# Kernel tuning notes

Measured on AMD Instinct MI355X. Metric: run time of the kernel, lower is better.

The kernel has to match this reference:

```python
import jax, jax.numpy as jnp
import numpy as np

D_MODEL = 1024
D_EXPERT = 1024
NUM_EXPERTS = 8
TOP_K = 2


def setup_inputs() -> dict:
    key = jax.random.key(0)
    k_x, k_r, k1, k2, k3 = jax.random.split(key, 5)
    scale = 0.02
    x = jax.random.normal(k_x, (4, 2048, D_MODEL), dtype=jnp.float32)
    Wr = jax.random.normal(k_r, (D_MODEL, NUM_EXPERTS), dtype=jnp.float32) * scale
    # stacked per-expert SwiGLU weights (Linear with bias=False)
    W1 = jax.random.normal(k1, (NUM_EXPERTS, D_MODEL, D_EXPERT), dtype=jnp.float32) * scale
    W2 = jax.random.normal(k2, (NUM_EXPERTS, D_EXPERT, D_MODEL), dtype=jnp.float32) * scale
    W3 = jax.random.normal(k3, (NUM_EXPERTS, D_MODEL, D_EXPERT), dtype=jnp.float32) * scale
    return {"x": x, "Wr": Wr, "W1": W1, "W2": W2, "W3": W3}


def reference(x, Wr, W1, W2, W3):
    B, T, C = x.shape
    xf = x.reshape(-1, C)                       # [N, C], N = B*T
    logits = xf @ Wr                            # [N, E]
    probs = jax.nn.softmax(logits, axis=-1)
    topk_p, topk_i = jax.lax.top_k(probs, TOP_K)  # [N, K]
    topk_p = topk_p / jnp.sum(topk_p, axis=-1, keepdims=True)
    out = jnp.zeros_like(xf)
    for e in range(NUM_EXPERTS):
        # combine weight per token for this expert (0 if not routed here)
        w_e = jnp.sum(topk_p * (topk_i == e), axis=-1)  # [N]
        h = jax.nn.silu(xf @ W1[e]) * (xf @ W3[e])       # [N, d_expert]
        y = h @ W2[e]                                    # [N, C]
        out = out + w_e[:, None] * y
    return out.reshape(B, T, C)
```

## Files before the change

### kernel.cpp

```cpp
#include <hip/hip_runtime.h>
#include <hip/hip_bf16.h>

typedef __attribute__((ext_vector_type(8))) short short8;
typedef __attribute__((ext_vector_type(4))) short short4v;
typedef __attribute__((ext_vector_type(4))) unsigned short ushort4v;
typedef __attribute__((ext_vector_type(4))) float f32x4;

#define NTOK 8192
#define DM 1024
#define DE 1024
#define NE 8

__device__ __forceinline__ float bf2f(unsigned short u) {
  union { unsigned int i; float f; } v; v.i = ((unsigned int)u) << 16; return v.f;
}
__device__ __forceinline__ unsigned short f2bf(float f) {
  union { float f; unsigned int i; } v; v.f = f;
  unsigned int lsb = (v.i >> 16) & 1;
  v.i += 0x7fffu + lsb;
  return (unsigned short)(v.i >> 16);
}
__device__ __forceinline__ void gl_lds(const short* g, short* l) {
  __builtin_amdgcn_global_load_lds((const __attribute__((address_space(1))) void*)g,
                                   (__attribute__((address_space(3))) void*)l, 16, 0, 0);
}

__global__ __launch_bounds__(256) void k_transw(const float* __restrict__ W1,
                                                const float* __restrict__ W2,
                                                const float* __restrict__ W3,
                                                short* __restrict__ wcat,
                                                short* __restrict__ w2t) {
  __shared__ float t[64][65];
  int mid = blockIdx.z;
  const float* src;
  if (mid < 8)       src = W1 + (size_t)mid * (DM * DE);
  else if (mid < 16) src = W3 + (size_t)(mid - 8) * (DM * DE);
  else               src = W2 + (size_t)(mid - 16) * (DE * DM);
  int tid = threadIdx.x;
  int tr = tid >> 4, tc = tid & 15;
  int kbase = blockIdx.y * 64, nbase = blockIdx.x * 64;
#pragma unroll
  for (int j = 0; j < 4; j++) {
    int kr = tr + j * 16;
    f32x4 v = *(const f32x4*)(src + (size_t)(kbase + kr) * 1024 + nbase + tc * 4);
    t[kr][tc * 4 + 0] = v[0]; t[kr][tc * 4 + 1] = v[1];
    t[kr][tc * 4 + 2] = v[2]; t[kr][tc * 4 + 3] = v[3];
  }
  __syncthreads();
#pragma unroll
  for (int j = 0; j < 4; j++) {
    int n = tr + j * 16;
    int ng = nbase + n;
    short4v o;
    o[0] = (short)f2bf(t[tc * 4 + 0][n]);
    o[1] = (short)f2bf(t[tc * 4 + 1][n]);
    o[2] = (short)f2bf(t[tc * 4 + 2][n]);
    o[3] = (short)f2bf(t[tc * 4 + 3][n]);
    size_t dsto;
    if (mid < 16) {
      int e = mid & 7, p = mid >> 3;
      int row_out = ((ng >> 7) * 256) + p * 128 + (ng & 127);
      dsto = (size_t)e * (2048 * 1024) + (size_t)row_out * 1024 + kbase + tc * 4;
      *(short4v*)(wcat + dsto) = o;
    } else {
      int e = mid - 16;
      dsto = (size_t)e * (1024 * 1024) + (size_t)ng * 1024 + kbase + tc * 4;
      *(short4v*)(w2t + dsto) = o;
    }
  }
}

__global__ __launch_bounds__(256) void k_router(const float* __restrict__ x,
                                                const float* __restrict__ Wr,
                                                short* __restrict__ xb,
                                                int* __restrict__ esel,
                                                float* __restrict__ wgt) {
  int wid = threadIdx.x >> 6, lane = threadIdx.x & 63;
  int t = blockIdx.x * 4 + wid;
  const float* xr = x + (size_t)t * DM;
  float acc[8];
#pragma unroll
  for (int e = 0; e < 8; e++) acc[e] = 0.f;
#pragma unroll
  for (int i = 0; i < 4; i++) {
    int kb = (i * 64 + lane) * 4;
    f32x4 v = *(const f32x4*)(xr + kb);
    ushort4v ob;
#pragma unroll
    for (int j = 0; j < 4; j++) {
      f32x4 w0 = *(const f32x4*)(Wr + (size_t)(kb + j) * 8);
      f32x4 w1 = *(const f32x4*)(Wr + (size_t)(kb + j) * 8 + 4);
      float xv = v[j];
      ob[j] = f2bf(xv);
      acc[0] += xv * w0[0]; acc[1] += xv * w0[1];
      acc[2] += xv * w0[2]; acc[3] += xv * w0[3];
      acc[4] += xv * w1[0]; acc[5] += xv * w1[1];
      acc[6] += xv * w1[2]; acc[7] += xv * w1[3];
    }
    *(ushort4v*)(xb + (size_t)t * DM + kb) = ob;
  }
#pragma unroll
  for (int off = 32; off; off >>= 1)
#pragma unroll
    for (int e = 0; e < 8; e++) acc[e] += __shfl_xor(acc[e], off);
  float m0 = -1e30f, m1 = -1e30f; int e0 = 0, e1 = 0;
#pragma unroll
  for (int e = 0; e < 8; e++) {
    float v = acc[e];
    if (v > m0) { m1 = m0; e1 = e0; m0 = v; e0 = e; }
    else if (v > m1) { m1 = v; e1 = e; }
  }
  float p = __expf(m1 - m0);
  if (lane == 0) {
    esel[2 * t] = e0; esel[2 * t + 1] = e1;
    wgt[2 * t] = 1.f / (1.f + p); wgt[2 * t + 1] = p / (1.f + p);
  }
}

__global__ __launch_bounds__(256) void k_rank(const int* __restrict__ esel,
                                              int* __restrict__ cnt,
                                              int* __restrict__ rank) {
  __shared__ int wcnt[4][8];
  __shared__ int woff[4][8];
  int tid = threadIdx.x;
  int lane = tid & 63, wid = tid >> 6;
  int t = blockIdx.x * 256 + tid;
  int e0 = esel[2 * t], e1 = esel[2 * t + 1];
  unsigned long long lt = (lane == 0) ? 0ull : ((~0ull) >> (64 - lane));
  int r0 = 0, r1 = 0;
#pragma unroll
  for (int e = 0; e < 8; e++) {
    unsigned long long m0 = __ballot(e0 == e);
    unsigned long long m1 = __ballot(e1 == e);
    int c0 = __popcll(m0);
    if (e0 == e) r0 = __popcll(m0 & lt);
    if (e1 == e) r1 = c0 + __popcll(m1 & lt);
    if (lane == 0) wcnt[wid][e] = c0 + __popcll(m1);
  }
  __syncthreads();
  if (tid < 8) {
    int e = tid;
    int c0 = wcnt[0][e], c1 = wcnt[1][e], c2 = wcnt[2][e], c3 = wcnt[3][e];
    int base = atomicAdd(&cnt[e], c0 + c1 + c2 + c3);
    woff[0][e] = base;
    woff[1][e] = base + c0;
    woff[2][e] = base + c0 + c1;
    woff[3][e] = base + c0 + c1 + c2;
  }
  __syncthreads();
  rank[2 * t] = woff[wid][e0] + r0;
  rank[2 * t + 1] = woff[wid][e1] + r1;
}

__global__ void k_offsets(const int* __restrict__ cnt, int* __restrict__ off) {
  if (threadIdx.x == 0) {
    int s = 0;
    for (int e = 0; e < NE; e++) { off[e] = s; s += cnt[e]; }
  }
}

__global__ __launch_bounds__(256) void k_scatter(const int* __restrict__ off,
                                                 const int* __restrict__ esel,
                                                 const int* __restrict__ rank,
                                                 int* __restrict__ tok_of_slot,
                                                 int* __restrict__ slot_of_tok) {
  int t = blockIdx.x * 256 + threadIdx.x;
#pragma unroll
  for (int j = 0; j < 2; j++) {
    int e = esel[2 * t + j];
    int s = off[e] + rank[2 * t + j];
    tok_of_slot[s] = t;
    slot_of_tok[2 * t + j] = s;
  }
}

template<int FFN1>
__global__ __launch_bounds__(512, 2) void k_ffn(const short* __restrict__ Abase,
                                                const short* __restrict__ Bbase,
                                                const int* __restrict__ cnt,
                                                const int* __restrict__ off,
                                                const int* __restrict__ tok_of_slot,
                                                short* __restrict__ outp) {
  const int e = blockIdx.y;
  const int cnt_e = cnt[e];
  const int m0 = blockIdx.z * 256;
  if (m0 >= cnt_e) return;
  const int bse = off[e];
  const int nt = blockIdx.x;
  const short* Bt = Bbase + (size_t)e * ((FFN1 ? 2048 : 1024) * 1024) + (size_t)(nt * 256) * 1024;

  __shared__ __align__(128) short Al[2][16384];
  __shared__ __align__(128) short Bl[2][16384];

  const int tid = threadIdx.x;
  const int lane = tid & 63, wid = tid >> 6;
  const int wr = wid >> 2, wcn = wid & 3;

  const short* srcA[4]; const short* srcB[4];
#pragma unroll
  for (int p = 0; p < 4; p++) {
    int r = p * 64 + (tid >> 3);
    int sc = (tid & 7) ^ (r & 7);
    int rowA = m0 + r; if (rowA >= cnt_e) rowA = cnt_e - 1;
    long ar = FFN1 ? (long)tok_of_slot[bse + rowA] : (long)(bse + rowA);
    srcA[p] = Abase + ar * 1024 + sc * 8;
    srcB[p] = Bt + (size_t)r * 1024 + sc * 8;
  }

  int aoff[8], boff[4];
#pragma unroll
  for (int m = 0; m < 8; m++) {
    int r = wr * 128 + m * 16 + (lane & 15);
    aoff[m] = r * 128 + (((lane >> 4) ^ (r & 7)) * 16);
  }
#pragma unroll
  for (int n = 0; n < 4; n++) {
    int rb = FFN1 ? (wcn * 32 + (n & 1) * 16 + (n >> 1) * 128 + (lane & 15))
                  : (wcn * 64 + n * 16 + (lane & 15));
    boff[n] = rb * 128 + (((lane >> 4) ^ (rb & 7)) * 16);
  }

  f32x4 acc[8][4];
#pragma unroll
  for (int m = 0; m < 8; m++)
#pragma unroll
    for (int n = 0; n < 4; n++) acc[m][n] = (f32x4){0.f, 0.f, 0.f, 0.f};

#pragma unroll
  for (int p = 0; p < 4; p++) gl_lds(srcA[p], &Al[0][p * 4096 + wid * 512]);
#pragma unroll
  for (int p = 0; p < 4; p++) gl_lds(srcB[p], &Bl[0][p * 4096 + wid * 512]);
  asm volatile("s_waitcnt vmcnt(0)" ::: "memory");
  __builtin_amdgcn_s_barrier();

  int cur = 0;
  for (int t = 0; t < 16; ++t) {
    const int nxt = cur ^ 1;
    const int ktn = (t + 1 < 16) ? (t + 1) : 15;
    const char* Ab = (const char*)Al[cur];
    const char* Bb = (const char*)Bl[cur];
    short8 a[4], b[4];
#pragma unroll
    for (int i = 0; i < 4; i++) a[i] = *(const short8*)(Ab + aoff[i]);
#pragma unroll
    for (int i = 0; i < 4; i++) b[i] = *(const short8*)(Bb + boff[i]);
#pragma unroll
    for (int p = 0; p < 4; p++) gl_lds(srcA[p] + ktn * 64, &Al[nxt][p * 4096 + wid * 512]);
    __builtin_amdgcn_s_setprio(1);
#pragma unroll
    for (int m = 0; m < 4; m++)
#pragma unroll
      for (int n = 0; n < 4; n++)
        acc[m][n] = __builtin_amdgcn_mfma_f32_16x16x32_bf16(a[m], b[n], acc[m][n], 0, 0, 0);
#pragma unroll
    for (int i = 0; i < 4; i++) a[i] = *(const short8*)(Ab + aoff[4 + i]);
#pragma unroll
    for (int p = 0; p < 4; p++) gl_lds(srcB[p] + ktn * 64, &Bl[nxt][p * 4096 + wid * 512]);
#pragma unroll
    for (int m = 0; m < 4; m++)
#pragma unroll
      for (int n = 0; n < 4; n++)
        acc[m + 4][n] = __builtin_amdgcn_mfma_f32_16x16x32_bf16(a[m], b[n], acc[m + 4][n], 0, 0, 0);
#pragma unroll
    for (int i = 0; i < 4; i++) a[i] = *(const short8*)(Ab + (aoff[i] ^ 64));
#pragma unroll
    for (int i = 0; i < 4; i++) b[i] = *(const short8*)(Bb + (boff[i] ^ 64));
#pragma unroll
    for (int m = 0; m < 4; m++)
#pragma unroll
      for (int n = 0; n < 4; n++)
        acc[m][n] = __builtin_amdgcn_mfma_f32_16x16x32_bf16(a[m], b[n], acc[m][n], 0, 0, 0);
#pragma unroll
    for (int i = 0; i < 4; i++) a[i] = *(const short8*)(Ab + (aoff[4 + i] ^ 64));
#pragma unroll
    for (int m = 0; m < 4; m++)
#pragma unroll
      for (int n = 0; n < 4; n++)
        acc[m + 4][n] = __builtin_amdgcn_mfma_f32_16x16x32_bf16(a[m], b[n], acc[m + 4][n], 0, 0, 0);
    __builtin_amdgcn_s_setprio(0);
    asm volatile("s_waitcnt vmcnt(0)" ::: "memory");
    __builtin_amdgcn_s_barrier();
    cur = nxt;
  }

  if (FFN1) {
#pragma unroll
    for (int m = 0; m < 8; m++)
#pragma unroll
      for (int cc = 0; cc < 2; cc++) {
        f32x4 v1 = acc[m][cc], v3 = acc[m][cc + 2];
        int col = nt * 128 + wcn * 32 + cc * 16 + (lane & 15);
#pragma unroll
        for (int i = 0; i < 4; i++) {
          int row = m0 + wr * 128 + m * 16 + ((lane >> 4) * 4) + i;
          if (row < cnt_e) {
            float a1v = v1[i];
            float hv = (a1v / (1.f + __expf(-a1v))) * v3[i];
            outp[(size_t)(bse + row) * DE + col] = (short)f2bf(hv);
          }
        }
      }
  } else {
#pragma unroll
    for (int m = 0; m < 8; m++)
#pragma unroll
      for (int n = 0; n < 4; n++) {
        f32x4 v = acc[m][n];
        int col = nt * 256 + wcn * 64 + n * 16 + (lane & 15);
#pragma unroll
        for (int i = 0; i < 4; i++) {
          int row = m0 + wr * 128 + m * 16 + ((lane >> 4) * 4) + i;
          if (row < cnt_e)
            outp[(size_t)(bse + row) * DM + col] = (short)f2bf(v[i]);
        }
      }
  }
}

__global__ __launch_bounds__(256) void k_combine(const short* __restrict__ y,
                                                 const int* __restrict__ slot_of_tok,
                                                 const float* __restrict__ wgt,
                                                 float* __restrict__ out) {
  int t = blockIdx.x;
  int s0 = slot_of_tok[2 * t], s1 = slot_of_tok[2 * t + 1];
  float w0 = wgt[2 * t], w1 = wgt[2 * t + 1];
  int c = threadIdx.x * 4;
  short4v a = *(const short4v*)(y + (size_t)s0 * DM + c);
  short4v b = *(const short4v*)(y + (size_t)s1 * DM + c);
  f32x4 o;
#pragma unroll
  for (int j = 0; j < 4; j++)
    o[j] = w0 * bf2f((unsigned short)a[j]) + w1 * bf2f((unsigned short)b[j]);
  *(f32x4*)(out + (size_t)t * DM + c) = o;
}

extern "C" void kernel_launch(void* const* d_in, const int* in_sizes, int n_in,
                              void* d_out, int out_size, void* d_ws, size_t ws_size,
                              hipStream_t stream) {
  const float* x  = (const float*)d_in[0];
  const float* Wr = (const float*)d_in[1];
  const float* W1 = (const float*)d_in[2];
  const float* W2 = (const float*)d_in[3];
  const float* W3 = (const float*)d_in[4];
  float* out = (float*)d_out;
  char* ws = (char*)d_ws;

  short* xb   = (short*)(ws);
  short* wcat = (short*)(ws + 16777216);
  short* w2t  = (short*)(ws + 50331648);
  short* h    = (short*)(ws + 67108864);
  short* y    = (short*)(ws + 100663296);
  char* meta = ws + 134217728;
  int* cnt          = (int*)(meta);
  int* off          = (int*)(meta + 256);
  int* esel         = (int*)(meta + 512);
  int* rank         = (int*)(meta + 512 + 65536);
  int* tok_of_slot  = (int*)(meta + 512 + 2 * 65536);
  int* slot_of_tok  = (int*)(meta + 512 + 3 * 65536);
  float* wgt        = (float*)(meta + 512 + 4 * 65536);

  hipMemsetAsync(cnt, 0, 32, stream);
  k_transw<<<dim3(16, 16, 24), 256, 0, stream>>>(W1, W2, W3, wcat, w2t);
  k_router<<<2048, 256, 0, stream>>>(x, Wr, xb, esel, wgt);
  k_rank<<<32, 256, 0, stream>>>(esel, cnt, rank);
  k_offsets<<<1, 64, 0, stream>>>(cnt, off);
  k_scatter<<<32, 256, 0, stream>>>(off, esel, rank, tok_of_slot, slot_of_tok);
  k_ffn<1><<<dim3(8, 8, 32), 512, 0, stream>>>(xb, wcat, cnt, off, tok_of_slot, h);
  k_ffn<0><<<dim3(4, 8, 32), 512, 0, stream>>>(h, w2t, cnt, off, tok_of_slot, y);
  k_combine<<<8192, 256, 0, stream>>>(y, slot_of_tok, wgt, out);
}
```

Baseline: 261.9 us.

## Split GEMM tiles into half-tile stages with finer-grained async LDS prefetch

Restructures the expert GEMM main loop so A and B tiles are loaded in halves, with partial vmcnt waits instead of a full drain each K-step. Loads for the next and next-next K-step are interleaved with MFMA blocks, and the first half-buffer is refilled as soon as it has been consumed. The warp-to-tile mapping is also interleaved (rows strided by 32 across warps, columns by 64), and the epilogue index math is updated to match. The aim is to hide global-to-LDS latency behind compute and keep the MFMA pipe busy. The cost is more barriers per step and careful vmcnt accounting that could race if miscounted.

```diff
diff --git a/kernel.cpp b/kernel.cpp
--- a/kernel.cpp
+++ b/kernel.cpp
@@ -196,29 +196,26 @@
   const int lane = tid & 63, wid = tid >> 6;
   const int wr = wid >> 2, wcn = wid & 3;
 
-  const short* srcA[4]; const short* srcB[4];
-#pragma unroll
-  for (int p = 0; p < 4; p++) {
-    int r = p * 64 + (tid >> 3);
-    int sc = (tid & 7) ^ (r & 7);
-    int rowA = m0 + r; if (rowA >= cnt_e) rowA = cnt_e - 1;
-    long ar = FFN1 ? (long)tok_of_slot[bse + rowA] : (long)(bse + rowA);
-    srcA[p] = Abase + ar * 1024 + sc * 8;
-    srcB[p] = Bt + (size_t)r * 1024 + sc * 8;
-  }
-
-  int aoff[8], boff[4];
-#pragma unroll
-  for (int m = 0; m < 8; m++) {
-    int r = wr * 128 + m * 16 + (lane & 15);
-    aoff[m] = r * 128 + (((lane >> 4) ^ (r & 7)) * 16);
-  }
-#pragma unroll
-  for (int n = 0; n < 4; n++) {
-    int rb = FFN1 ? (wcn * 32 + (n & 1) * 16 + (n >> 1) * 128 + (lane & 15))
-                  : (wcn * 64 + n * 16 + (lane & 15));
-    boff[n] = rb * 128 + (((lane >> 4) ^ (rb & 7)) * 16);
-  }
+  const int sc = ((lane & 7) ^ (lane >> 3)) * 8;
+  const short* srcA[2][2];
+  const short* srcB[2];
+#pragma unroll
+  for (int j = 0; j < 2; j++) {
+#pragma unroll
+    for (int h = 0; h < 2; h++) {
+      int r = h * 128 + (wid * 2 + j) * 8 + (lane >> 3);
+      int row = m0 + r; if (row >= cnt_e) row = cnt_e - 1;
+      long ar = FFN1 ? (long)tok_of_slot[bse + row] : (long)(bse + row);
+      srcA[j][h] = Abase + ar * 1024 + sc;
+    }
+    srcB[j] = Bt + (size_t)((wid * 2 + j) * 8 + (lane >> 3)) * 1024 + sc;
+  }
+
+  const int chnk = ((lane >> 4) ^ (lane & 7)) * 16;
+  const int aB0 = (wr * 16 + (lane & 15)) * 128 + chnk;
+  const int aB1 = aB0 ^ 64;
+  const int bB0 = (wcn * 16 + (lane & 15)) * 128 + chnk;
+  const int bB1 = bB0 ^ 64;
 
   f32x4 acc[8][4];
 #pragma unroll
@@ -226,73 +223,78 @@
 #pragma unroll
     for (int n = 0; n < 4; n++) acc[m][n] = (f32x4){0.f, 0.f, 0.f, 0.f};
 
-#pragma unroll
-  for (int p = 0; p < 4; p++) gl_lds(srcA[p], &Al[0][p * 4096 + wid * 512]);
-#pragma unroll
-  for (int p = 0; p < 4; p++) gl_lds(srcB[p], &Bl[0][p * 4096 + wid * 512]);
+#define STG_A(b, h, kt) { \
+    gl_lds(srcA[0][h] + (kt) * 64, &Al[b][(h) * 8192 + (wid * 2 + 0) * 512]); \
+    gl_lds(srcA[1][h] + (kt) * 64, &Al[b][(h) * 8192 + (wid * 2 + 1) * 512]); }
+#define STG_B(b, h, kt) { \
+    gl_lds(srcB[0] + (h) * 131072 + (kt) * 64, &Bl[b][(h) * 8192 + (wid * 2 + 0) * 512]); \
+    gl_lds(srcB[1] + (h) * 131072 + (kt) * 64, &Bl[b][(h) * 8192 + (wid * 2 + 1) * 512]); }
+
+  STG_A(0, 0, 0); STG_B(0, 0, 0); STG_B(0, 1, 0); STG_A(0, 1, 0);
+  STG_A(1, 0, 1); STG_B(1, 0, 1);
+
+#define KTBODY(KT, BUF) { \
+    const int kA = ((KT) + 1 < 16) ? (KT) + 1 : 15; \
+    const int kB = ((KT) + 2 < 16) ? (KT) + 2 : 15; \
+    const char* pA = (const char*)(&Al[BUF][0]); \
+    const char* pB = (const char*)(&Bl[BUF][0]); \
+    short8 a[4], b0[4], b1[4]; \
+     \
+    asm volatile("s_waitcnt vmcnt(6)" ::: "memory"); \
+    __builtin_amdgcn_s_barrier(); \
+    _Pragma("unroll") for (int m = 0; m < 4; m++) a[m] = *(const short8*)(pA + aB0 + m * 4096); \
+    _Pragma("unroll") for (int n = 0; n < 4; n++) b0[n] = *(const short8*)(pB + bB0 + (n & 1) * 8192 + (n >> 1) * 16384); \
+    STG_B(BUF ^ 1, 1, kA); \
+    __builtin_amdgcn_s_setprio(1); \
+    _Pragma("unroll") for (int m = 0; m < 4; m++) \
+      _Pragma("unroll") for (int n = 0; n < 4; n++) \
+        acc[m][n] = __builtin_amdgcn_mfma_f32_16x16x32_bf16(a[m], b0[n], acc[m][n], 0, 0, 0); \
+    __builtin_amdgcn_s_setprio(0); \
+     \
+    _Pragma("unroll") for (int m = 0; m < 4; m++) a[m] = *(const short8*)(pA + aB1 + m * 4096); \
+    _Pragma("unroll") for (int n = 0; n < 4; n++) b1[n] = *(const short8*)(pB + bB1 + (n & 1) * 8192 + (n >> 1) * 16384); \
+    STG_A(BUF ^ 1, 1, kA); \
+    __builtin_amdgcn_s_setprio(1); \
+    _Pragma("unroll") for (int m = 0; m < 4; m++) \
+      _Pragma("unroll") for (int n = 0; n < 4; n++) \
+        acc[m][n] = __builtin_amdgcn_mfma_f32_16x16x32_bf16(a[m], b1[n], acc[m][n], 0, 0, 0); \
+    __builtin_amdgcn_s_setprio(0); \
+     \
+    asm volatile("s_waitcnt vmcnt(8)" ::: "memory"); \
+    __builtin_amdgcn_s_barrier(); \
+    _Pragma("unroll") for (int m = 0; m < 4; m++) a[m] = *(const short8*)(pA + aB0 + 16384 + m * 4096); \
+    STG_A(BUF, 0, kB); \
+    __builtin_amdgcn_s_setprio(1); \
+    _Pragma("unroll") for (int m = 0; m < 4; m++) \
+      _Pragma("unroll") for (int n = 0; n < 4; n++) \
+        acc[m + 4][n] = __builtin_amdgcn_mfma_f32_16x16x32_bf16(a[m], b0[n], acc[m + 4][n], 0, 0, 0); \
+    __builtin_amdgcn_s_setprio(0); \
+     \
+    _Pragma("unroll") for (int m = 0; m < 4; m++) a[m] = *(const short8*)(pA + aB1 + 16384 + m * 4096); \
+    STG_B(BUF, 0, kB); \
+    __builtin_amdgcn_s_setprio(1); \
+    _Pragma("unroll") for (int m = 0; m < 4; m++) \
+      _Pragma("unroll") for (int n = 0; n < 4; n++) \
+        acc[m + 4][n] = __builtin_amdgcn_mfma_f32_16x16x32_bf16(a[m], b1[n], acc[m + 4][n], 0, 0, 0); \
+    __builtin_amdgcn_s_setprio(0); \
+  }
+
+  for (int kt2 = 0; kt2 < 16; kt2 += 2) {
+    KTBODY(kt2, 0);
+    KTBODY(kt2 + 1, 1);
+  }
   asm volatile("s_waitcnt vmcnt(0)" ::: "memory");
-  __builtin_amdgcn_s_barrier();
-
-  int cur = 0;
-  for (int t = 0; t < 16; ++t) {
-    const int nxt = cur ^ 1;
-    const int ktn = (t + 1 < 16) ? (t + 1) : 15;
-    const char* Ab = (const char*)Al[cur];
-    const char* Bb = (const char*)Bl[cur];
-    short8 a[4], b[4];
-#pragma unroll
-    for (int i = 0; i < 4; i++) a[i] = *(const short8*)(Ab + aoff[i]);
-#pragma unroll
-    for (int i = 0; i < 4; i++) b[i] = *(const short8*)(Bb + boff[i]);
-#pragma unroll
-    for (int p = 0; p < 4; p++) gl_lds(srcA[p] + ktn * 64, &Al[nxt][p * 4096 + wid * 512]);
-    __builtin_amdgcn_s_setprio(1);
-#pragma unroll
-    for (int m = 0; m < 4; m++)
-#pragma unroll
-      for (int n = 0; n < 4; n++)
-        acc[m][n] = __builtin_amdgcn_mfma_f32_16x16x32_bf16(a[m], b[n], acc[m][n], 0, 0, 0);
-#pragma unroll
-    for (int i = 0; i < 4; i++) a[i] = *(const short8*)(Ab + aoff[4 + i]);
-#pragma unroll
-    for (int p = 0; p < 4; p++) gl_lds(srcB[p] + ktn * 64, &Bl[nxt][p * 4096 + wid * 512]);
-#pragma unroll
-    for (int m = 0; m < 4; m++)
-#pragma unroll
-      for (int n = 0; n < 4; n++)
-        acc[m + 4][n] = __builtin_amdgcn_mfma_f32_16x16x32_bf16(a[m], b[n], acc[m + 4][n], 0, 0, 0);
-#pragma unroll
-    for (int i = 0; i < 4; i++) a[i] = *(const short8*)(Ab + (aoff[i] ^ 64));
-#pragma unroll
-    for (int i = 0; i < 4; i++) b[i] = *(const short8*)(Bb + (boff[i] ^ 64));
-#pragma unroll
-    for (int m = 0; m < 4; m++)
-#pragma unroll
-      for (int n = 0; n < 4; n++)
-        acc[m][n] = __builtin_amdgcn_mfma_f32_16x16x32_bf16(a[m], b[n], acc[m][n], 0, 0, 0);
-#pragma unroll
-    for (int i = 0; i < 4; i++) a[i] = *(const short8*)(Ab + (aoff[4 + i] ^ 64));
-#pragma unroll
-    for (int m = 0; m < 4; m++)
-#pragma unroll
-      for (int n = 0; n < 4; n++)
-        acc[m + 4][n] = __builtin_amdgcn_mfma_f32_16x16x32_bf16(a[m], b[n], acc[m + 4][n], 0, 0, 0);
-    __builtin_amdgcn_s_setprio(0);
-    asm volatile("s_waitcnt vmcnt(0)" ::: "memory");
-    __builtin_amdgcn_s_barrier();
-    cur = nxt;
-  }
 
   if (FFN1) {
 #pragma unroll
     for (int m = 0; m < 8; m++)
 #pragma unroll
-      for (int cc = 0; cc < 2; cc++) {
-        f32x4 v1 = acc[m][cc], v3 = acc[m][cc + 2];
-        int col = nt * 128 + wcn * 32 + cc * 16 + (lane & 15);
+      for (int n = 0; n < 2; n++) {
+        f32x4 v1 = acc[m][n], v3 = acc[m][n + 2];
+        int col = nt * 128 + n * 64 + wcn * 16 + (lane & 15);
 #pragma unroll
         for (int i = 0; i < 4; i++) {
-          int row = m0 + wr * 128 + m * 16 + ((lane >> 4) * 4) + i;
+          int row = m0 + (m >> 2) * 128 + (m & 3) * 32 + wr * 16 + ((lane >> 4) * 4) + i;
           if (row < cnt_e) {
             float a1v = v1[i];
             float hv = (a1v / (1.f + __expf(-a1v))) * v3[i];
@@ -306,10 +308,10 @@
 #pragma unroll
       for (int n = 0; n < 4; n++) {
         f32x4 v = acc[m][n];
-        int col = nt * 256 + wcn * 64 + n * 16 + (lane & 15);
+        int col = nt * 256 + (n >> 1) * 128 + (n & 1) * 64 + wcn * 16 + (lane & 15);
 #pragma unroll
         for (int i = 0; i < 4; i++) {
-          int row = m0 + wr * 128 + m * 16 + ((lane >> 4) * 4) + i;
+          int row = m0 + (m >> 2) * 128 + (m & 3) * 32 + wr * 16 + ((lane >> 4) * 4) + i;
           if (row < cnt_e)
             outp[(size_t)(bse + row) * DM + col] = (short)f2bf(v[i]);
         }
```

New measurement: 253.7 us. 1.03x faster.
